# Kernel tuning notes

Measured on AMD Instinct MI355X. Metric: run time of the kernel, lower is better.

The kernel has to match this reference:

```python
import jax, jax.numpy as jnp
import numpy as np

B, K, D, V = 8192, 32, 128, 2048
WEIGHT, SIGMA, NDCG_K = 0.15, 1.0, 10
N = K + 1


def _to_hyperboloid(x):
    # lift spatial coords onto Lorentz hyperboloid: x0 = sqrt(1 + ||x||^2)
    t = jnp.sqrt(1.0 + jnp.sum(x * x, axis=-1, keepdims=True))
    return jnp.concatenate([t, x], axis=-1)


def _lorentz_dist(u, v):
    # d(u,v) = arccosh(-<u,v>_L), <u,v>_L = -u0*v0 + u[1:].v[1:]
    inner = -u[..., 0] * v[..., 0] + jnp.sum(u[..., 1:] * v[..., 1:], axis=-1)
    return jnp.arccosh(jnp.maximum(-inner, 1.0 + 1e-7))


def setup_inputs() -> dict:
    key = jax.random.key(0)
    k = jax.random.split(key, 7)
    anchor_emb = _to_hyperboloid(jax.random.normal(k[0], (B, D), dtype=jnp.float32))
    positive_emb = _to_hyperboloid(jax.random.normal(k[1], (B, D), dtype=jnp.float32))
    negative_embs = _to_hyperboloid(jax.random.normal(k[2], (B * K, D), dtype=jnp.float32))
    tree_distances = jax.random.uniform(k[3], (V, V), dtype=jnp.float32) * 10.0
    anchor_idx = jax.random.randint(k[4], (B,), 0, V, dtype=jnp.int32)
    pos_idx = jax.random.randint(k[5], (B,), 0, V, dtype=jnp.int32)
    neg_idx = jax.random.randint(k[6], (B, K), 0, V, dtype=jnp.int32)
    return {"anchor_emb": anchor_emb, "positive_emb": positive_emb,
            "negative_embs": negative_embs, "tree_distances": tree_distances,
            "anchor_idx": anchor_idx, "pos_idx": pos_idx, "neg_idx": neg_idx}


def _lambdarank(anchor_emb, positive_emb, negative_embs, tree_distances,
                anchor_idx, pos_idx, neg_idx):
    neg = negative_embs.reshape(B, K, -1)
    pos_dist = _lorentz_dist(anchor_emb, positive_emb)            # (B,)
    neg_dists = _lorentz_dist(anchor_emb[:, None, :], neg)        # (B,K)
    d = jnp.concatenate([pos_dist[:, None], neg_dists], axis=1)   # (B,N)

    pos_t = tree_distances[anchor_idx, pos_idx]                   # (B,)
    neg_t = tree_distances[anchor_idx[:, None], neg_idx]          # (B,K)
    t = jnp.concatenate([pos_t[:, None], neg_t], axis=1)          # (B,N)
    max_t = jnp.max(t, axis=1, keepdims=True)
    rel = (max_t - t + 1e-6) / (max_t + 1e-6)                     # (B,N)

    k_top = min(NDCG_K, N)
    # 1-based rank of each item under ascending-distance sort (piecewise const)
    ranks = jnp.argsort(jnp.argsort(d, axis=1), axis=1) + 1       # (B,N)
    disc = jnp.where(ranks <= k_top,
                     1.0 / jnp.log2(ranks.astype(jnp.float32) + 1.0), 0.0)
    ideal = -jnp.sort(-rel, axis=1)[:, :k_top]                    # (B,k)
    log_pos = jnp.log2(jnp.arange(2, k_top + 2, dtype=jnp.float32))
    idcg = jnp.sum(ideal / log_pos, axis=1)                       # (B,)

    # closed-form |delta NDCG| of swapping items i,j in the ranking:
    # |(rel_i - rel_j) * (disc_i - disc_j)| / IDCG
    drel = rel[:, :, None] - rel[:, None, :]                      # (B,N,N)
    ddisc = disc[:, :, None] - disc[:, None, :]
    inv_idcg = jnp.where(idcg > 0, 1.0 / idcg, 0.0)[:, None, None]
    delta = jnp.abs(drel * ddisc) * inv_idcg

    # lambda_ij = sign(rel_i-rel_j) * delta * sigmoid(sign * sigma * (d_j - d_i))
    S = jnp.sign(drel)
    dd = d[:, None, :] - d[:, :, None]                            # d_j - d_i
    lam = S * delta * jax.nn.sigmoid(S * SIGMA * dd)
    # loss = sum_{i<j} lam_ij*(d_i-d_j); antisymmetric -> 0.5 * full sum
    loss_b = 0.5 * jnp.sum(lam * (-dd), axis=(1, 2))              # (B,)
    return WEIGHT * jnp.mean(loss_b)


def reference(anchor_emb, positive_emb, negative_embs, tree_distances,
              anchor_idx, pos_idx, neg_idx):
    return _lambdarank(anchor_emb, positive_emb, negative_embs, tree_distances,
                       anchor_idx, pos_idx, neg_idx)
```

## Files before the change

kernel.cpp:

```cpp
#include <hip/hip_runtime.h>
#include <math.h>

#define BB 8192
#define KK 32
#define DD 129
#define VV 2048
#define NN 33
#define TOPK 10

__device__ __forceinline__ float fast_rcp(float x) { return __builtin_amdgcn_rcpf(x); }

__global__ __launch_bounds__(256) void lr_main(
    const float* __restrict__ anchor,
    const float* __restrict__ positive,
    const float* __restrict__ neg,
    const float* __restrict__ tree,
    const int* __restrict__ a_idx,
    const int* __restrict__ p_idx,
    const int* __restrict__ n_idx,
    float* __restrict__ partial)
{
    __shared__ float  sA[DD];
    __shared__ float  sP[DD];
    __shared__ float  sR[KK * DD];
    __shared__ float  st_[NN];
    __shared__ float  sd[NN];
    __shared__ float4 sitem[NN];
    __shared__ float  sinv;
    __shared__ float  swave[4];

    const int b    = blockIdx.x;
    const int t    = threadIdx.x;
    const int wave = t >> 6;
    const int lane = t & 63;
    const int g    = lane >> 4;
    const int subl = lane & 15;

    {
        const float4* g4 = (const float4*)(neg + (size_t)b * (KK * DD));
        float4* s4 = (float4*)sR;
        #pragma unroll
        for (int c = 0; c < 5; ++c) {
            int i = c * 256 + t;
            if (i < (KK * DD) / 4) s4[i] = g4[i];
        }
    }
    if (t < DD) {
        sA[t] = anchor[(size_t)b * DD + t];
        sP[t] = positive[(size_t)b * DD + t];
    }
    if (t < NN) {
        int ai = a_idx[b];
        st_[t] = (t == 0)
            ? tree[(size_t)ai * VV + p_idx[b]]
            : tree[(size_t)ai * VV + n_idx[(size_t)b * KK + (t - 1)]];
    }
    __syncthreads();

    {
        float areg[8];
        #pragma unroll
        for (int e = 0; e < 8; ++e) areg[e] = sA[e * 16 + subl];
        const float a128 = sA[128];
        const float a0   = sA[0];

        #pragma unroll
        for (int round = 0; round < 3; ++round) {
            int row = round * 16 + wave * 4 + g;
            if (row < NN) {
                const float* r = (row == 0) ? sP : (sR + (row - 1) * DD);
                float s = 0.0f;
                #pragma unroll
                for (int e = 0; e < 8; ++e) s = fmaf(areg[e], r[e * 16 + subl], s);
                s += __shfl_xor(s, 8, 64);
                s += __shfl_xor(s, 4, 64);
                s += __shfl_xor(s, 2, 64);
                s += __shfl_xor(s, 1, 64);
                if (subl == 0) {
                    float full = s + a128 * r[128];
                    float x = fmaxf(2.0f * a0 * r[0] - full, 1.0f + 1e-07f);
                    sd[row] = __logf(x + sqrtf(x * x - 1.0f));
                }
            }
        }
    }
    __syncthreads();

    if (t < NN) {
        float maxt = st_[0];
        #pragma unroll
        for (int j = 1; j < NN; ++j) maxt = fmaxf(maxt, st_[j]);
        float rel = (maxt - st_[t] + 1e-06f) * fast_rcp(maxt + 1e-06f);

        float di = sd[t];
        int cnt = 0;
        #pragma unroll
        for (int j = 0; j < NN; ++j) {
            float dj = sd[j];
            cnt += (int)((dj < di) | ((dj == di) & (j < t)));
        }
        int rank = cnt + 1;
        float disc = (rank <= TOPK) ? fast_rcp(log2f((float)(rank + 1))) : 0.0f;
        sitem[t] = make_float4(di, rel, disc, 0.0f);
    }
    __syncthreads();

    if (wave == 0) {
        float c = 0.0f;
        if (t < NN) {
            float ri = sitem[t].y;
            int pos = 0;
            #pragma unroll
            for (int j = 0; j < NN; ++j) {
                float rj = sitem[j].y;
                pos += (int)((rj > ri) | ((rj == ri) & (j < t)));
            }
            if (pos < TOPK) c = ri * fast_rcp(log2f((float)(pos + 2)));
        }
        #pragma unroll
        for (int off = 32; off > 0; off >>= 1) c += __shfl_xor(c, off, 64);
        if (t == 0) sinv = (c > 0.0f) ? fast_rcp(c) : 0.0f;
    }
    __syncthreads();

    float acc = 0.0f;
    {
        const float inv = sinv;
        #pragma unroll
        for (int c = 0; c < 5; ++c) {
            int p = c * 256 + t;
            if (p < NN * NN) {
                int i = p / NN;
                int j = p - i * NN;
                float4 Ii = sitem[i];
                float4 Ij = sitem[j];
                float dd    = Ij.x - Ii.x;
                float drel  = Ii.y - Ij.y;
                float ddisc = Ii.z - Ij.z;
                float t1  = drel * fabsf(ddisc) * inv;
                float e   = __expf(-dd);
                float num = (drel >= 0.0f) ? 1.0f : e;
                acc = fmaf(t1 * num * fast_rcp(1.0f + e), -dd, acc);
            }
        }
    }
    #pragma unroll
    for (int off = 32; off > 0; off >>= 1) acc += __shfl_xor(acc, off, 64);
    if (lane == 0) swave[wave] = acc;
    __syncthreads();
    if (t == 0)
        partial[b] = 0.5f * (swave[0] + swave[1] + swave[2] + swave[3]);
}

__global__ __launch_bounds__(256) void lr_reduce(
    const float* __restrict__ partial, float* __restrict__ out)
{
    __shared__ float swave[4];
    const float4* p4 = (const float4*)partial;
    float acc = 0.0f;
    #pragma unroll
    for (int c = 0; c < (BB / 4) / 256; ++c) {
        float4 v = p4[c * 256 + threadIdx.x];
        acc += (v.x + v.y) + (v.z + v.w);
    }
    #pragma unroll
    for (int off = 32; off > 0; off >>= 1) acc += __shfl_xor(acc, off, 64);
    if ((threadIdx.x & 63) == 0) swave[threadIdx.x >> 6] = acc;
    __syncthreads();
    if (threadIdx.x == 0)
        out[0] = (swave[0] + swave[1] + swave[2] + swave[3]) * (0.15f / (float)BB);
}

extern "C" void kernel_launch(void* const* d_in, const int* in_sizes, int n_in,
                              void* d_out, int out_size, void* d_ws, size_t ws_size,
                              hipStream_t stream)
{
    const float* anchor   = (const float*)d_in[0];
    const float* positive = (const float*)d_in[1];
    const float* neg      = (const float*)d_in[2];
    const float* tree     = (const float*)d_in[3];
    const int*   a_idx    = (const int*)d_in[4];
    const int*   p_idx    = (const int*)d_in[5];
    const int*   n_idx    = (const int*)d_in[6];
    float* partial = (float*)d_ws;

    lr_main<<<BB, 256, 0, stream>>>(anchor, positive, neg, tree,
                                    a_idx, p_idx, n_idx, partial);
    lr_reduce<<<1, 256, 0, stream>>>(partial, (float*)d_out);
}
```

Measured before the change: 237.3 us.

## Map one wave per batch row and load rows directly into registers

Each 256-thread block now handles four batch rows, one per wave, instead of one row per block. The negatives, positive and anchor rows are loaded straight from global memory into registers rather than staged through a 16KB shared buffer, and the IDCG reduction uses wave shuffles in place of a block-level broadcast. This removes the large shared-memory footprint and several block barriers, which should raise occupancy and shorten per-row latency. The cost is much higher register pressure from the 9x8 value array, plus a 33x33 pair loop that now runs 17 iterations per lane with some out-of-range indices.

```diff
diff --git a/kernel.cpp b/kernel.cpp
--- a/kernel.cpp
+++ b/kernel.cpp
@@ -7,10 +7,11 @@
 #define VV 2048
 #define NN 33
 #define TOPK 10
+#define WPB 4
 
 __device__ __forceinline__ float fast_rcp(float x) { return __builtin_amdgcn_rcpf(x); }
 
-__global__ __launch_bounds__(256) void lr_main(
+__global__ __launch_bounds__(256) void lr_fused(
     const float* __restrict__ anchor,
     const float* __restrict__ positive,
     const float* __restrict__ neg,
@@ -20,136 +21,120 @@
     const int* __restrict__ n_idx,
     float* __restrict__ partial)
 {
-    __shared__ float  sA[DD];
-    __shared__ float  sP[DD];
-    __shared__ float  sR[KK * DD];
-    __shared__ float  st_[NN];
-    __shared__ float  sd[NN];
-    __shared__ float4 sitem[NN];
-    __shared__ float  sinv;
-    __shared__ float  swave[4];
+    __shared__ float  st_[WPB][NN];
+    __shared__ float  sd_[WPB][NN];
+    __shared__ float4 sitem[WPB][NN];
 
-    const int b    = blockIdx.x;
     const int t    = threadIdx.x;
     const int wave = t >> 6;
     const int lane = t & 63;
     const int g    = lane >> 4;
     const int subl = lane & 15;
+    const int b    = blockIdx.x * WPB + wave;
 
-    {
-        const float4* g4 = (const float4*)(neg + (size_t)b * (KK * DD));
-        float4* s4 = (float4*)sR;
+    const int ai  = a_idx[b];
+    const int col = (lane == 0) ? p_idx[b]
+                                : n_idx[(size_t)b * KK + ((lane < NN ? lane : KK) - 1)];
+    const float tg = tree[(size_t)ai * VV + col];
+
+    const float* ab = anchor   + (size_t)b * DD;
+    const float* pb = positive + (size_t)b * DD;
+    const float* nb = neg      + (size_t)b * (KK * DD);
+
+    float areg[8];
+    #pragma unroll
+    for (int e = 0; e < 8; ++e) areg[e] = ab[e * 16 + subl];
+    const float a128 = ab[128];
+
+    const float* rp[9];
+    #pragma unroll
+    for (int r = 0; r < 9; ++r) {
+        int row = 4 * r + g;
+        if (row > KK) row = KK;
+        rp[r] = (row == 0) ? pb : (nb + (size_t)(row - 1) * DD);
+    }
+    float vv[9][8];
+    #pragma unroll
+    for (int r = 0; r < 9; ++r)
         #pragma unroll
-        for (int c = 0; c < 5; ++c) {
-            int i = c * 256 + t;
-            if (i < (KK * DD) / 4) s4[i] = g4[i];
-        }
-    }
-    if (t < DD) {
-        sA[t] = anchor[(size_t)b * DD + t];
-        sP[t] = positive[(size_t)b * DD + t];
-    }
-    if (t < NN) {
-        int ai = a_idx[b];
-        st_[t] = (t == 0)
-            ? tree[(size_t)ai * VV + p_idx[b]]
-            : tree[(size_t)ai * VV + n_idx[(size_t)b * KK + (t - 1)]];
-    }
-    __syncthreads();
+        for (int e = 0; e < 8; ++e)
+            vv[r][e] = rp[r][e * 16 + subl];
+    float t128[9];
+    #pragma unroll
+    for (int r = 0; r < 9; ++r) t128[r] = rp[r][128];
 
-    {
-        float areg[8];
+    if (lane < NN) st_[wave][lane] = tg;
+
+    #pragma unroll
+    for (int r = 0; r < 9; ++r) {
+        float s = 0.0f;
         #pragma unroll
-        for (int e = 0; e < 8; ++e) areg[e] = sA[e * 16 + subl];
-        const float a128 = sA[128];
-        const float a0   = sA[0];
-
-        #pragma unroll
-        for (int round = 0; round < 3; ++round) {
-            int row = round * 16 + wave * 4 + g;
-            if (row < NN) {
-                const float* r = (row == 0) ? sP : (sR + (row - 1) * DD);
-                float s = 0.0f;
-                #pragma unroll
-                for (int e = 0; e < 8; ++e) s = fmaf(areg[e], r[e * 16 + subl], s);
-                s += __shfl_xor(s, 8, 64);
-                s += __shfl_xor(s, 4, 64);
-                s += __shfl_xor(s, 2, 64);
-                s += __shfl_xor(s, 1, 64);
-                if (subl == 0) {
-                    float full = s + a128 * r[128];
-                    float x = fmaxf(2.0f * a0 * r[0] - full, 1.0f + 1e-07f);
-                    sd[row] = __logf(x + sqrtf(x * x - 1.0f));
-                }
-            }
+        for (int e = 0; e < 8; ++e) s = fmaf(areg[e], vv[r][e], s);
+        s += __shfl_xor(s, 8, 64);
+        s += __shfl_xor(s, 4, 64);
+        s += __shfl_xor(s, 2, 64);
+        s += __shfl_xor(s, 1, 64);
+        int row = 4 * r + g;
+        if (subl == 0 && row < NN) {
+            float full = s + a128 * t128[r];
+            float x = fmaxf(fmaf(2.0f * areg[0], vv[r][0], -full), 1.0f + 1e-07f);
+            sd_[wave][row] = __logf(x + sqrtf(x * x - 1.0f));
         }
     }
     __syncthreads();
 
-    if (t < NN) {
-        float maxt = st_[0];
+    if (lane < NN) {
+        float maxt = st_[wave][0];
         #pragma unroll
-        for (int j = 1; j < NN; ++j) maxt = fmaxf(maxt, st_[j]);
-        float rel = (maxt - st_[t] + 1e-06f) * fast_rcp(maxt + 1e-06f);
+        for (int j = 1; j < NN; ++j) maxt = fmaxf(maxt, st_[wave][j]);
+        float rel = (maxt - st_[wave][lane] + 1e-06f) * fast_rcp(maxt + 1e-06f);
 
-        float di = sd[t];
+        float di = sd_[wave][lane];
         int cnt = 0;
         #pragma unroll
         for (int j = 0; j < NN; ++j) {
-            float dj = sd[j];
-            cnt += (int)((dj < di) | ((dj == di) & (j < t)));
+            float dj = sd_[wave][j];
+            cnt += (int)((dj < di) | ((dj == di) & (j < lane)));
         }
-        int rank = cnt + 1;
-        float disc = (rank <= TOPK) ? fast_rcp(log2f((float)(rank + 1))) : 0.0f;
-        sitem[t] = make_float4(di, rel, disc, 0.0f);
+        float disc = (cnt + 1 <= TOPK) ? fast_rcp(log2f((float)(cnt + 2))) : 0.0f;
+        sitem[wave][lane] = make_float4(di, rel, disc, 0.0f);
     }
     __syncthreads();
 
-    if (wave == 0) {
-        float c = 0.0f;
-        if (t < NN) {
-            float ri = sitem[t].y;
-            int pos = 0;
-            #pragma unroll
-            for (int j = 0; j < NN; ++j) {
-                float rj = sitem[j].y;
-                pos += (int)((rj > ri) | ((rj == ri) & (j < t)));
-            }
-            if (pos < TOPK) c = ri * fast_rcp(log2f((float)(pos + 2)));
+    float c = 0.0f;
+    if (lane < NN) {
+        float ri = sitem[wave][lane].y;
+        int pos = 0;
+        #pragma unroll
+        for (int j = 0; j < NN; ++j) {
+            float rj = sitem[wave][j].y;
+            pos += (int)((rj > ri) | ((rj == ri) & (j < lane)));
         }
-        #pragma unroll
-        for (int off = 32; off > 0; off >>= 1) c += __shfl_xor(c, off, 64);
-        if (t == 0) sinv = (c > 0.0f) ? fast_rcp(c) : 0.0f;
+        if (pos < TOPK) c = ri * fast_rcp(log2f((float)(pos + 2)));
     }
-    __syncthreads();
+    #pragma unroll
+    for (int off = 32; off > 0; off >>= 1) c += __shfl_xor(c, off, 64);
+    const float inv = (c > 0.0f) ? fast_rcp(c) : 0.0f;
 
     float acc = 0.0f;
-    {
-        const float inv = sinv;
-        #pragma unroll
-        for (int c = 0; c < 5; ++c) {
-            int p = c * 256 + t;
-            if (p < NN * NN) {
-                int i = p / NN;
-                int j = p - i * NN;
-                float4 Ii = sitem[i];
-                float4 Ij = sitem[j];
-                float dd    = Ij.x - Ii.x;
-                float drel  = Ii.y - Ij.y;
-                float ddisc = Ii.z - Ij.z;
-                float t1  = drel * fabsf(ddisc) * inv;
-                float e   = __expf(-dd);
-                float num = (drel >= 0.0f) ? 1.0f : e;
-                acc = fmaf(t1 * num * fast_rcp(1.0f + e), -dd, acc);
-            }
-        }
+    #pragma unroll
+    for (int it = 0; it < 17; ++it) {
+        int p = it * 64 + lane;
+        int i = p / NN;
+        int j = p - i * NN;
+        float4 Ii = sitem[wave][i];
+        float4 Ij = sitem[wave][j];
+        float dd    = Ij.x - Ii.x;
+        float drel  = Ii.y - Ij.y;
+        float ddisc = Ii.z - Ij.z;
+        float t1  = drel * fabsf(ddisc) * inv;
+        float e   = __expf(-dd);
+        float num = (drel >= 0.0f) ? 1.0f : e;
+        acc = fmaf(t1 * num * fast_rcp(1.0f + e), -dd, acc);
     }
     #pragma unroll
     for (int off = 32; off > 0; off >>= 1) acc += __shfl_xor(acc, off, 64);
-    if (lane == 0) swave[wave] = acc;
-    __syncthreads();
-    if (t == 0)
-        partial[b] = 0.5f * (swave[0] + swave[1] + swave[2] + swave[3]);
+    if (lane == 0) partial[b] = 0.5f * acc;
 }
 
 __global__ __launch_bounds__(256) void lr_reduce(
@@ -184,7 +169,7 @@
     const int*   n_idx    = (const int*)d_in[6];
     float* partial = (float*)d_ws;
 
-    lr_main<<<BB, 256, 0, stream>>>(anchor, positive, neg, tree,
-                                    a_idx, p_idx, n_idx, partial);
+    lr_fused<<<BB / WPB, 256, 0, stream>>>(anchor, positive, neg, tree,
+                                           a_idx, p_idx, n_idx, partial);
     lr_reduce<<<1, 256, 0, stream>>>(partial, (float*)d_out);
 }
```

After: 224.5 us. 5.4% less time.
